# Performance work log

Measured on AMD Instinct MI355X. Metric: run time of the kernel, lower is better.

Reference implementation:

```python
import jax, jax.numpy as jnp
import numpy as np

K = 16  # top-k neighbors (init kwarg k)
EPS = 1e-8


def setup_inputs() -> dict:
    key = jax.random.key(0)
    # bs=8, closeness=12, flows=2, N=2048
    x_c = jax.random.normal(key, (8, 12, 2, 2048), dtype=jnp.float32)
    return {"x_c": x_c, "flow": 0}


def _cosine_adjacency(x):
    # x: (bs, 2, N, closeness) -> per-node feature = concat of both flows over time
    bs, f, N, c = x.shape
    feats = jnp.transpose(x, (0, 2, 1, 3)).reshape(bs, N, f * c)  # (bs, N, 2*closeness)
    fn = feats / (jnp.linalg.norm(feats, axis=-1, keepdims=True) + EPS)
    return jnp.einsum('bnd,bmd->bnm', fn, fn)  # (bs, N, N)


def reference(x_c, flow):
    # x_c: (bs, closeness, 2, N)
    bs, closeness, _, N = x_c.shape
    x = jnp.transpose(x_c, (0, 2, 3, 1)).astype(jnp.float32)  # (bs, 2, N, closeness)

    # mode == 'cos': cosine-similarity adjacency
    A = _cosine_adjacency(x)

    # index = argsort(A, descending)[:, :, :k]  ==  top-k neighbor indices per node
    _, index = jax.lax.top_k(A, K)  # (bs, N, K)

    # batched gather replacing the bs x N python double loop:
    # sx_c[i, j] = x[i, flow, index[i, j]]
    x_flow = x[:, flow]  # (bs, N, closeness)
    sx_c = jax.vmap(lambda xf, idx: xf[idx])(x_flow, index)  # (bs, N, K, closeness)

    # tgt_mode == 'c': tgt = x[:, flow].unsqueeze(-2)  -> (bs, N, 1, closeness)
    tgt = x_flow[:, :, None, :]
    # returned as tgt.permute(0,2,3,1).squeeze(1) -> (bs, closeness, N)
    tgt_out = jnp.squeeze(jnp.transpose(tgt, (0, 2, 3, 1)), axis=1)

    return sx_c, tgt_out
```

## Files before the change

kernel.cpp:

```cpp
#include <hip/hip_runtime.h>
#include <hip/hip_bf16.h>
#include <math.h>

#define BS   8
#define NPTS 2048
#define CCH  12
#define NF   2
#define DIM  24
#define KPAD 32
#define KTOP 16
#define NWV  8
#define RPB  16
#define CBUF 112
#define CBS  113
#define WVS  20

#define NROWS    (BS * NPTS)
#define TGT_BASE (NROWS * KTOP * CCH)

typedef unsigned long long u64;
typedef unsigned int       u32;
typedef unsigned short     u16;
typedef __attribute__((ext_vector_type(8))) short short8;
typedef __attribute__((ext_vector_type(4))) float f32x4;

#define WS_FEATS 0
#define WS_RAW   (NROWS * DIM * 4)
#define WS_FHI   (WS_RAW + NROWS * CCH * 4)
#define WS_FLO   (WS_FHI + NROWS * KPAD * 2)

__device__ __forceinline__ float np_norm_den(const float* __restrict__ v)
{
#pragma clang fp contract(off)
    float s[DIM];
    #pragma unroll
    for (int d = 0; d < DIM; ++d) s[d] = v[d] * v[d];
    float r[8];
    #pragma unroll
    for (int j = 0; j < 8; ++j) r[j] = (s[j] + s[j + 8]) + s[j + 16];
    float res = ((r[0] + r[1]) + (r[2] + r[3])) + ((r[4] + r[5]) + (r[6] + r[7]));
    return sqrtf(res) + 1e-8f;
}

__device__ __forceinline__ u32 ordf(float f)
{
    u32 u = __float_as_uint(f);
    return ((int)u >= 0) ? (u | 0x80000000u) : ~u;
}

__device__ __forceinline__ u16 bf16_rne(float x)
{
    u32 bits = __float_as_uint(x);
    bits += 0x7fffu + ((bits >> 16) & 1u);
    return (u16)(bits >> 16);
}

__global__ __launch_bounds__(64) void prep_kernel(
    const float* __restrict__ x_c,
    const int*   __restrict__ flow_p,
    float*       __restrict__ feats,
    u16*         __restrict__ fhi,
    u16*         __restrict__ flo,
    float*       __restrict__ raw,
    float*       __restrict__ out)
{
    const int t = blockIdx.x * 64 + threadIdx.x;
    const int b = t >> 11;
    const int n = t & (NPTS - 1);
    const float* xb = x_c + (size_t)b * CCH * NF * NPTS;

    float v[DIM];
    float fn[DIM];
    {
#pragma clang fp contract(off)
        #pragma unroll
        for (int c = 0; c < CCH; ++c)
            #pragma unroll
            for (int f = 0; f < NF; ++f)
                v[f * CCH + c] = xb[(c * NF + f) * NPTS + n];

        const float den = np_norm_den(v);
        float* fo = feats + (size_t)t * DIM;
        #pragma unroll
        for (int d = 0; d < DIM; ++d) { fn[d] = v[d] / den; fo[d] = fn[d]; }
    }

    u16* ho = fhi + (size_t)t * KPAD;
    u16* lo = flo + (size_t)t * KPAD;
    #pragma unroll
    for (int d = 0; d < DIM; ++d) {
        const u16 hb = bf16_rne(fn[d]);
        const float hf = __uint_as_float((u32)hb << 16);
        ho[d] = hb;
        lo[d] = bf16_rne(fn[d] - hf);
    }
    #pragma unroll
    for (int d = DIM; d < KPAD; ++d) { ho[d] = 0; lo[d] = 0; }

    const int flow = flow_p[0];
    float* ro = raw + (size_t)t * CCH;
    #pragma unroll
    for (int c = 0; c < CCH; ++c) {
        const float xv = flow ? v[CCH + c] : v[c];
        ro[c] = xv;
        out[TGT_BASE + ((size_t)b * CCH + c) * NPTS + n] = xv;
    }
}

#define CLEANUP_DESC(arr)                                         \
    _Pragma("unroll")                                             \
    for (int j_ = 8; j_ > 0; j_ >>= 1)                            \
        _Pragma("unroll")                                         \
        for (int i_ = 0; i_ < KTOP; ++i_) {                       \
            const int l_ = i_ | j_;                               \
            if (l_ > i_) {                                        \
                const float a_ = arr[i_], c_ = arr[l_];           \
                arr[i_] = fmaxf(a_, c_);                          \
                arr[l_] = fminf(a_, c_);                          \
            }                                                     \
        }

#define APPROX_TILE(ACC, AHI, ALO, BHI, BLO)                                  \
    f32x4 ACC  = {0.0f, 0.0f, 0.0f, 0.0f};                                    \
    {                                                                         \
        f32x4 acc2_ = {0.0f, 0.0f, 0.0f, 0.0f};                               \
        ACC   = __builtin_amdgcn_mfma_f32_16x16x32_bf16(AHI, BHI, ACC, 0,0,0);\
        acc2_ = __builtin_amdgcn_mfma_f32_16x16x32_bf16(AHI, BLO, acc2_,0,0,0);\
        ACC   = __builtin_amdgcn_mfma_f32_16x16x32_bf16(ALO, BHI, ACC, 0,0,0);\
        _Pragma("unroll")                                                     \
        for (int i_ = 0; i_ < 4; ++i_) ACC[i_] += acc2_[i_];                  \
    }

__global__ __launch_bounds__(512, 6) void fused_topk_kernel(
    const float* __restrict__ feats,
    const u16*   __restrict__ fhi,
    const u16*   __restrict__ flo,
    const float* __restrict__ raw,
    float*       __restrict__ out)
{
    __shared__ union {
        float wval[NWV * 16 * WVS];
        float vk[NWV * KTOP * 16];
        u64   ckey[RPB * CBS];
    } sh;
    __shared__ float thr_s[RPB];
    __shared__ int   cnt[RPB];
    __shared__ int   sel[RPB][KTOP];

    const int tid  = threadIdx.x;
    const int lane = tid & 63;
    const int w    = __builtin_amdgcn_readfirstlane(tid >> 6);
    const int b     = blockIdx.x >> 7;
    const int chunk = blockIdx.x & 127;
    const int rb    = chunk * RPB;
    const int p     = lane & 15;
    const int q     = lane >> 4;

    if (tid < RPB) cnt[tid] = 0;

    short8 ahi, alo;
    {
        const size_t ae = ((size_t)(b * NPTS + rb + p)) * KPAD + q * 8;
        ahi = *(const short8*)(fhi + ae);
        alo = *(const short8*)(flo + ae);
    }

    float* wv = sh.wval + w * (16 * WVS);

    float vlist[KTOP];
    #pragma unroll
    for (int k = 0; k < KTOP; ++k) vlist[k] = -3.0f;

    for (int ro = 0; ro < 2; ++ro) {
        float bv[16];
        #pragma unroll
        for (int t = 0; t < 4; ++t) {
            const int cb0 = w * 128 + ro * 64 + t * 16;
            const size_t be = ((size_t)(b * NPTS + cb0 + p)) * KPAD + q * 8;
            const short8 bhi = *(const short8*)(fhi + be);
            const short8 blo = *(const short8*)(flo + be);
            APPROX_TILE(acc, ahi, alo, bhi, blo)
            *(f32x4*)(wv + p * WVS + q * 4) = acc;
            #pragma unroll
            for (int i = 0; i < 4; ++i)
                bv[t * 4 + i] = wv[(q * 4 + i) * WVS + p];
        }
        #pragma unroll
        for (int k = 2; k <= 16; k <<= 1)
            #pragma unroll
            for (int j = k >> 1; j > 0; j >>= 1)
                #pragma unroll
                for (int i = 0; i < 16; ++i) {
                    const int l = i | j;
                    if (l > i) {
                        const float a = bv[i], c = bv[l];
                        if ((i & k) == 0) { bv[i] = fminf(a, c); bv[l] = fmaxf(a, c); }
                        else              { bv[i] = fmaxf(a, c); bv[l] = fminf(a, c); }
                    }
                }
        #pragma unroll
        for (int i = 0; i < 16; ++i) vlist[i] = fmaxf(vlist[i], bv[i]);
        CLEANUP_DESC(vlist)
    }

    #pragma unroll
    for (int x = 16; x <= 32; x <<= 1) {
        float other[KTOP];
        #pragma unroll
        for (int k = 0; k < KTOP; ++k) other[k] = __shfl_xor(vlist[k], x);
        #pragma unroll
        for (int i = 0; i < KTOP; ++i)
            vlist[i] = fmaxf(vlist[i], other[KTOP - 1 - i]);
        CLEANUP_DESC(vlist)
    }

    __syncthreads();

    for (int half = NWV / 2; half >= 1; half >>= 1) {
        if (w >= half && w < 2 * half && q == 0) {
            #pragma unroll
            for (int k = 0; k < KTOP; ++k)
                sh.vk[(w * KTOP + k) * 16 + p] = vlist[k];
        }
        __syncthreads();
        if (w < half) {
            float other[KTOP];
            #pragma unroll
            for (int k = 0; k < KTOP; ++k)
                other[k] = sh.vk[((w + half) * KTOP + k) * 16 + p];
            #pragma unroll
            for (int i = 0; i < KTOP; ++i)
                vlist[i] = fmaxf(vlist[i], other[KTOP - 1 - i]);
            CLEANUP_DESC(vlist)
        }
        __syncthreads();
    }
    if (w == 0 && q == 0) thr_s[p] = vlist[KTOP - 1] - 8e-4f;
    __syncthreads();

    float thrv[4];
    #pragma unroll
    for (int i = 0; i < 4; ++i) thrv[i] = thr_s[q * 4 + i];

    {
        size_t be_n = ((size_t)(b * NPTS + w * 256 + p)) * KPAD + q * 8;
        short8 nbhi = *(const short8*)(fhi + be_n);
        short8 nblo = *(const short8*)(flo + be_n);
        for (int t = 0; t < 16; ++t) {
            const int cb0 = w * 256 + t * 16;
            const short8 bhi = nbhi, blo = nblo;
            if (t < 15) {
                const size_t be = ((size_t)(b * NPTS + cb0 + 16 + p)) * KPAD + q * 8;
                nbhi = *(const short8*)(fhi + be);
                nblo = *(const short8*)(flo + be);
            }
            APPROX_TILE(acc, ahi, alo, bhi, blo)
            #pragma unroll
            for (int i = 0; i < 4; ++i) {
                if (acc[i] >= thrv[i]) {
                    const int r = q * 4 + i;
                    const int pos = atomicAdd(&cnt[r], 1);
                    if (pos < CBUF)
                        sh.ckey[r * CBS + pos] = (u64)(u32)(cb0 + p);
                }
            }
        }
    }
    __syncthreads();

    {
        const int r = tid & 15;
        const float* fr = feats + (size_t)(b * NPTS + rb + r) * DIM;
        float rfn[DIM];
        #pragma unroll
        for (int d = 0; d < DIM; ++d) rfn[d] = fr[d];
        const int e = (cnt[r] < CBUF) ? cnt[r] : CBUF;
        for (int pos = tid >> 4; pos < e; pos += 32) {
            const int idx = (int)(u32)sh.ckey[r * CBS + pos];
            const float* cp = feats + (size_t)(b * NPTS + idx) * DIM;
            float acc = 0.0f;
            #pragma unroll
            for (int d = 0; d < DIM; ++d)
                acc = __builtin_fmaf(cp[d], rfn[d], acc);
            sh.ckey[r * CBS + pos] = ((u64)ordf(acc) << 32) | (u32)(2047 - idx);
        }
    }
    __syncthreads();

    {
        const int L = tid >> 5;
        const int g = tid & 31;
        const int e = (cnt[L] < CBUF) ? cnt[L] : CBUF;
        const u64* rowbuf = &sh.ckey[L * CBS];
        for (int pos = g; pos < e; pos += 32) {
            const u64 key = rowbuf[pos];
            int rank = 0;
            for (int p2 = 0; p2 < e; ++p2) rank += (rowbuf[p2] > key);
            if (rank < KTOP) sel[L][rank] = 2047 - (int)(key & 0xFFFFFFFFull);
        }
    }
    __syncthreads();

    const int rg = b * NPTS + rb;
    for (int e2 = tid; e2 < RPB * KTOP * CCH; e2 += 512) {
        const int L = e2 / (KTOP * CCH);
        const int r = e2 % (KTOP * CCH);
        const int k = r / CCH;
        const int c = r % CCH;
        out[((size_t)(rg + L) * KTOP + k) * CCH + c] =
            raw[((size_t)b * NPTS + sel[L][k]) * CCH + c];
    }
}

extern "C" void kernel_launch(void* const* d_in, const int* in_sizes, int n_in,
                              void* d_out, int out_size, void* d_ws, size_t ws_size,
                              hipStream_t stream)
{
    const float* x_c    = (const float*)d_in[0];
    const int*   flow_p = (const int*)d_in[1];
    float*       out    = (float*)d_out;

    float* feats = (float*)((char*)d_ws + WS_FEATS);
    float* raw   = (float*)((char*)d_ws + WS_RAW);
    u16*   fhi   = (u16*)  ((char*)d_ws + WS_FHI);
    u16*   flo   = (u16*)  ((char*)d_ws + WS_FLO);

    prep_kernel<<<NROWS / 64, 64, 0, stream>>>(x_c, flow_p, feats, fhi, flo, raw, out);
    fused_topk_kernel<<<BS * 128, 512, 0, stream>>>(feats, fhi, flo, raw, out);
}
```

Measured before the change: 105.8 us.

## Vectorize stores/loads, flatten cross-wave top-k merge, drop occupancy hint

The prep kernel now writes normalized features, bf16 hi/lo splits and raw flow values with 16-byte vector stores instead of scalar ones, and the rescoring loop loads candidate features as float4. In the top-k kernel the first sorted chunk seeds the running list directly, and the three-step shared-memory tree reduction across waves becomes a single exchange plus shuffle merges inside wave 0, which saves two barriers. The minimum-occupancy hint is removed from launch bounds, so the compiler may use more registers at the cost of fewer resident waves.

```diff
diff --git a/kernel.cpp b/kernel.cpp
--- a/kernel.cpp
+++ b/kernel.cpp
@@ -80,31 +80,45 @@
                 v[f * CCH + c] = xb[(c * NF + f) * NPTS + n];
 
         const float den = np_norm_den(v);
-        float* fo = feats + (size_t)t * DIM;
-        #pragma unroll
-        for (int d = 0; d < DIM; ++d) { fn[d] = v[d] / den; fo[d] = fn[d]; }
-    }
+        #pragma unroll
+        for (int d = 0; d < DIM; ++d) fn[d] = v[d] / den;
+    }
+
+    float* fo = feats + (size_t)t * DIM;
+    #pragma unroll
+    for (int j = 0; j < 6; ++j)
+        *(f32x4*)(fo + 4 * j) = *(f32x4*)(fn + 4 * j);
+
+    u16 hb[KPAD], lb[KPAD];
+    #pragma unroll
+    for (int d = 0; d < DIM; ++d) {
+        const u16 h = bf16_rne(fn[d]);
+        const float hf = __uint_as_float((u32)h << 16);
+        hb[d] = h;
+        lb[d] = bf16_rne(fn[d] - hf);
+    }
+    #pragma unroll
+    for (int d = DIM; d < KPAD; ++d) { hb[d] = 0; lb[d] = 0; }
 
     u16* ho = fhi + (size_t)t * KPAD;
     u16* lo = flo + (size_t)t * KPAD;
     #pragma unroll
-    for (int d = 0; d < DIM; ++d) {
-        const u16 hb = bf16_rne(fn[d]);
-        const float hf = __uint_as_float((u32)hb << 16);
-        ho[d] = hb;
-        lo[d] = bf16_rne(fn[d] - hf);
-    }
-    #pragma unroll
-    for (int d = DIM; d < KPAD; ++d) { ho[d] = 0; lo[d] = 0; }
+    for (int j = 0; j < 4; ++j) {
+        *(short8*)(ho + 8 * j) = ((const short8*)hb)[j];
+        *(short8*)(lo + 8 * j) = ((const short8*)lb)[j];
+    }
 
     const int flow = flow_p[0];
+    float rv[CCH];
+    #pragma unroll
+    for (int c = 0; c < CCH; ++c) {
+        rv[c] = flow ? v[CCH + c] : v[c];
+        out[TGT_BASE + ((size_t)b * CCH + c) * NPTS + n] = rv[c];
+    }
     float* ro = raw + (size_t)t * CCH;
     #pragma unroll
-    for (int c = 0; c < CCH; ++c) {
-        const float xv = flow ? v[CCH + c] : v[c];
-        ro[c] = xv;
-        out[TGT_BASE + ((size_t)b * CCH + c) * NPTS + n] = xv;
-    }
+    for (int j = 0; j < 3; ++j)
+        *(f32x4*)(ro + 4 * j) = *(f32x4*)(rv + 4 * j);
 }
 
 #define CLEANUP_DESC(arr)                                         \
@@ -131,7 +145,7 @@
         for (int i_ = 0; i_ < 4; ++i_) ACC[i_] += acc2_[i_];                  \
     }
 
-__global__ __launch_bounds__(512, 6) void fused_topk_kernel(
+__global__ __launch_bounds__(512) void fused_topk_kernel(
     const float* __restrict__ feats,
     const u16*   __restrict__ fhi,
     const u16*   __restrict__ flo,
@@ -167,12 +181,7 @@
 
     float* wv = sh.wval + w * (16 * WVS);
 
-    float vlist[KTOP];
-    #pragma unroll
-    for (int k = 0; k < KTOP; ++k) vlist[k] = -3.0f;
-
-    for (int ro = 0; ro < 2; ++ro) {
-        float bv[16];
+    auto gather_sorted16 = [&](int ro, float bv[16]) {
         #pragma unroll
         for (int t = 0; t < 4; ++t) {
             const int cb0 = w * 128 + ro * 64 + t * 16;
@@ -198,6 +207,15 @@
                         else              { bv[i] = fmaxf(a, c); bv[l] = fminf(a, c); }
                     }
                 }
+    };
+
+    float vlist[KTOP];
+    {
+        float bv[16];
+        gather_sorted16(0, bv);
+        #pragma unroll
+        for (int i = 0; i < 16; ++i) vlist[i] = bv[15 - i];
+        gather_sorted16(1, bv);
         #pragma unroll
         for (int i = 0; i < 16; ++i) vlist[i] = fmaxf(vlist[i], bv[i]);
         CLEANUP_DESC(vlist)
@@ -216,26 +234,35 @@
 
     __syncthreads();
 
-    for (int half = NWV / 2; half >= 1; half >>= 1) {
-        if (w >= half && w < 2 * half && q == 0) {
-            #pragma unroll
-            for (int k = 0; k < KTOP; ++k)
-                sh.vk[(w * KTOP + k) * 16 + p] = vlist[k];
-        }
-        __syncthreads();
-        if (w < half) {
+    if (q == 0) {
+        #pragma unroll
+        for (int k = 0; k < KTOP; ++k)
+            sh.vk[(w * KTOP + k) * 16 + p] = vlist[k];
+    }
+    __syncthreads();
+    if (w == 0) {
+        float la[KTOP], lb[KTOP];
+        #pragma unroll
+        for (int k = 0; k < KTOP; ++k) {
+            la[k] = sh.vk[(q * KTOP + k) * 16 + p];
+            lb[k] = sh.vk[((q + 4) * KTOP + k) * 16 + p];
+        }
+        #pragma unroll
+        for (int i = 0; i < KTOP; ++i)
+            la[i] = fmaxf(la[i], lb[KTOP - 1 - i]);
+        CLEANUP_DESC(la)
+        #pragma unroll
+        for (int x = 16; x <= 32; x <<= 1) {
             float other[KTOP];
             #pragma unroll
-            for (int k = 0; k < KTOP; ++k)
-                other[k] = sh.vk[((w + half) * KTOP + k) * 16 + p];
+            for (int k = 0; k < KTOP; ++k) other[k] = __shfl_xor(la[k], x);
             #pragma unroll
             for (int i = 0; i < KTOP; ++i)
-                vlist[i] = fmaxf(vlist[i], other[KTOP - 1 - i]);
-            CLEANUP_DESC(vlist)
-        }
-        __syncthreads();
-    }
-    if (w == 0 && q == 0) thr_s[p] = vlist[KTOP - 1] - 8e-4f;
+                la[i] = fmaxf(la[i], other[KTOP - 1 - i]);
+            CLEANUP_DESC(la)
+        }
+        if (q == 0) thr_s[p] = la[KTOP - 1] - 8e-4f;
+    }
     __syncthreads();
 
     float thrv[4];
@@ -273,15 +300,20 @@
         const float* fr = feats + (size_t)(b * NPTS + rb + r) * DIM;
         float rfn[DIM];
         #pragma unroll
-        for (int d = 0; d < DIM; ++d) rfn[d] = fr[d];
+        for (int j = 0; j < 6; ++j)
+            *(f32x4*)(rfn + 4 * j) = *(const f32x4*)(fr + 4 * j);
         const int e = (cnt[r] < CBUF) ? cnt[r] : CBUF;
         for (int pos = tid >> 4; pos < e; pos += 32) {
             const int idx = (int)(u32)sh.ckey[r * CBS + pos];
             const float* cp = feats + (size_t)(b * NPTS + idx) * DIM;
+            float cv[DIM];
+            #pragma unroll
+            for (int j = 0; j < 6; ++j)
+                *(f32x4*)(cv + 4 * j) = *(const f32x4*)(cp + 4 * j);
             float acc = 0.0f;
             #pragma unroll
             for (int d = 0; d < DIM; ++d)
-                acc = __builtin_fmaf(cp[d], rfn[d], acc);
+                acc = __builtin_fmaf(cv[d], rfn[d], acc);
             sh.ckey[r * CBS + pos] = ((u64)ordf(acc) << 32) | (u32)(2047 - idx);
         }
     }
```

Result: no change. 103.9 us (-1.8%).
